# Kernel tuning notes

Hardware: AMD Instinct MI355X
Metric: run time of the kernel (lower is better)

Reference implementation:

```python
import jax, jax.numpy as jnp
from jax import lax
import numpy as np


def tropical_conv1d(x, w, padding, mode):
    """Tropical semiring conv1d.
    y[b,o,t] = sum_c reduce_k ( x[b,c,t+k] + w[o,c,k] )
    where reduce is min (min-plus) or max (max-plus). Zero padding like nn.Conv1d.
    x: [B, C, L], w: [O, C, K] -> y: [B, O, L + 2p - K + 1]
    """
    if padding:
        x = jnp.pad(x, ((0, 0), (0, 0), (padding, padding)))
    B, C, L = x.shape
    O, _, K = w.shape
    Lo = L - K + 1
    big = jnp.array(np.inf if mode == 'min' else -np.inf, dtype=x.dtype)
    acc0 = jnp.full((B, O, C, Lo), big, dtype=x.dtype)
    red = jnp.minimum if mode == 'min' else jnp.maximum
    wk_all = jnp.moveaxis(w, 2, 0)          # [K, O, C]
    ks = jnp.arange(K)

    def step(acc, inp):
        k, wk = inp
        xs = lax.dynamic_slice_in_dim(x, k, Lo, axis=2)      # [B, C, Lo]
        v = xs[:, None, :, :] + wk[None, :, :, None]          # [B, O, C, Lo]
        return red(acc, v), None

    acc, _ = lax.scan(step, acc0, (ks, wk_all))
    return acc.sum(axis=2)                                    # [B, O, Lo]


def avg_pool1d_2(x):
    # avg_pool1d(kernel=2, stride=2), truncating odd tail like torch
    B, C, L = x.shape
    Lh = L // 2
    return x[..., : Lh * 2].reshape(B, C, Lh, 2).mean(axis=-1)


def setup_inputs() -> dict:
    key = jax.random.key(0)
    ks = jax.random.split(key, 9)
    B, Cin, L = 64, 3, 8192
    linear_size = 32448
    s = lambda k, shape, fan: jax.random.normal(k, shape, dtype=jnp.float32) * (1.0 / np.sqrt(fan))
    return {
        'input': jax.random.normal(ks[0], (B, Cin, L), dtype=jnp.float32),
        'w1': s(ks[1], (6, Cin, 80), Cin * 80),
        'w2': s(ks[2], (16, 6, 3), 6 * 3),
        'fc1_w': s(ks[3], (120, linear_size), linear_size),
        'fc1_b': jnp.zeros((120,), jnp.float32),
        'fc2_w': s(ks[4], (84, 120), 120),
        'fc2_b': jnp.zeros((84,), jnp.float32),
        'fc3_w': s(ks[5], (10, 84), 84),
        'fc3_b': jnp.zeros((10,), jnp.float32),
    }


def reference(input, w1, w2, fc1_w, fc1_b, fc2_w, fc2_b, fc3_w, fc3_b):
    x = tropical_conv1d(input, w1, padding=2, mode='min')   # [B,6,L-75]
    x = avg_pool1d_2(x)
    x = tropical_conv1d(x, w2, padding=0, mode='max')       # [B,16,L2]
    x = avg_pool1d_2(x)
    x = x.reshape(x.shape[0], -1)                            # [B, 16*floor(L2/2)]
    x = jax.nn.relu(x @ fc1_w.T + fc1_b)
    x = jax.nn.relu(x @ fc2_w.T + fc2_b)
    return x @ fc3_w.T + fc3_b
```

## Files before the change

### kernel.cpp

```cpp
#include <hip/hip_runtime.h>

#define BB 64
#define C1 3
#define LIN 8192
#define PAD1 2
#define O1 6
#define KK1 80
#define LP1 4058

#define O2 16
#define KK2 3
#define LP2 2028

#define NFLAT 32448
#define H1 120
#define H2 84
#define NOUT 10

typedef _Float16 h2 __attribute__((ext_vector_type(2)));
typedef _Float16 f16x8 __attribute__((ext_vector_type(8)));
typedef float f32x4 __attribute__((ext_vector_type(4)));
#define BIGH ((_Float16)30000.0f)

__device__ __forceinline__ h2 bch2(float f) { return __builtin_bit_cast(h2, f); }
__device__ __forceinline__ h2 mkB(float nxt, float cur) {
  unsigned lo = __builtin_bit_cast(unsigned, cur);
  unsigned hi = __builtin_bit_cast(unsigned, nxt);
  return __builtin_bit_cast(h2, (lo >> 16) | (hi << 16));
}

__global__ __launch_bounds__(256) void k_prep(const float* __restrict__ w1,
                                              float* __restrict__ whb) {
  const int idx = threadIdx.x + blockIdx.x * 256;
  if (idx >= (O1 * C1) * (KK1 / 2)) return;
  const int oc = idx / (KK1 / 2);
  const int m  = idx - oc * (KK1 / 2);
  h2 v;
  v.x = (_Float16)w1[oc * KK1 + 2 * m];
  v.y = (_Float16)w1[oc * KK1 + 2 * m + 1];
  whb[idx] = __builtin_bit_cast(float, v);
}

#define TJ1 256
#define NT1 16
#define DWIN 297
#define DPAD 304

__global__ __launch_bounds__(512, 8) void k_conv1(const float* __restrict__ x,
                                                  const float* __restrict__ whb,
                                                  float* __restrict__ p1) {
  __shared__ float As[C1][DPAD];
  __shared__ float ws[O1 * C1 * 40];
  const int b    = blockIdx.x >> 4;
  const int tile = blockIdx.x & 15;
  const int j0   = tile * TJ1;
  const int tid  = threadIdx.x;

  for (int idx = tid; idx < O1 * C1 * 40; idx += 512) ws[idx] = whb[idx];
  for (int q = tid; q < C1 * DWIN; q += 512) {
    const int c = q / DWIN;
    const int d = q - c * DWIN;
    const int E = 2 * (j0 + d) - PAD1;
    const float* xc = x + ((size_t)b * C1 + c) * LIN;
    float f0 = 0.f, f1 = 0.f;
    if ((unsigned)E < LIN) f0 = xc[E];
    if ((unsigned)(E + 1) < LIN) f1 = xc[E + 1];
    h2 A; A.x = (_Float16)f0; A.y = (_Float16)f1;
    As[c][d] = __builtin_bit_cast(float, A);
  }
  __syncthreads();

  const int og = tid >> 8;
  const int jj = tid & 255;
  const int ob = og * 3;

  float r0 = 0.f, r1 = 0.f, r2 = 0.f;

  for (int c = 0; c < C1; ++c) {
    h2 aA[3], aB[3];
#pragma unroll
    for (int oo = 0; oo < 3; ++oo) {
      aA[oo].x = BIGH; aA[oo].y = BIGH;
      aB[oo].x = BIGH; aB[oo].y = BIGH;
    }
    float4 cur = *(const float4*)&As[c][jj];
#pragma unroll 2
    for (int mq = 0; mq < 10; ++mq) {
      float4 nxt = *(const float4*)&As[c][jj + 4 * mq + 4];
      h2 A0 = bch2(cur.x), A1 = bch2(cur.y), A2 = bch2(cur.z), A3 = bch2(cur.w);
      h2 B0 = mkB(cur.y, cur.x);
      h2 B1 = mkB(cur.z, cur.y);
      h2 B2 = mkB(cur.w, cur.z);
      h2 B3 = mkB(nxt.x, cur.w);
#pragma unroll
      for (int oo = 0; oo < 3; ++oo) {
        float4 wq = *(const float4*)&ws[((ob + oo) * C1 + c) * 40 + 4 * mq];
        h2 w0 = bch2(wq.x), w1v = bch2(wq.y), w2v = bch2(wq.z), w3v = bch2(wq.w);
        aA[oo] = __builtin_elementwise_min(aA[oo], A0 + w0);
        aB[oo] = __builtin_elementwise_min(aB[oo], B0 + w0);
        aA[oo] = __builtin_elementwise_min(aA[oo], A1 + w1v);
        aB[oo] = __builtin_elementwise_min(aB[oo], B1 + w1v);
        aA[oo] = __builtin_elementwise_min(aA[oo], A2 + w2v);
        aB[oo] = __builtin_elementwise_min(aB[oo], B2 + w2v);
        aA[oo] = __builtin_elementwise_min(aA[oo], A3 + w3v);
        aB[oo] = __builtin_elementwise_min(aB[oo], B3 + w3v);
      }
      cur = nxt;
    }
    r0 += fminf((float)aA[0].x, (float)aA[0].y) + fminf((float)aB[0].x, (float)aB[0].y);
    r1 += fminf((float)aA[1].x, (float)aA[1].y) + fminf((float)aB[1].x, (float)aB[1].y);
    r2 += fminf((float)aA[2].x, (float)aA[2].y) + fminf((float)aB[2].x, (float)aB[2].y);
  }

  const int j = j0 + jj;
  if (j < LP1) {
    float* pb = p1 + (size_t)b * O1 * LP1 + j;
    pb[(ob + 0) * LP1] = 0.5f * r0;
    pb[(ob + 1) * LP1] = 0.5f * r1;
    pb[(ob + 2) * LP1] = 0.5f * r2;
  }
}

#define T2 256
#define XT2 516

__global__ __launch_bounds__(256) void k_conv2(const float* __restrict__ p1,
                                               const float* __restrict__ w2,
                                               _Float16* __restrict__ p2h) {
  __shared__ float ps[O1][XT2];
  __shared__ float w2s[O2 * O1 * KK2];
  const int b    = blockIdx.x >> 3;
  const int tile = blockIdx.x & 7;
  const int j0   = tile * T2;
  const int tid  = threadIdx.x;

  for (int idx = tid; idx < O2 * O1 * KK2; idx += 256) w2s[idx] = w2[idx];
  for (int idx = tid; idx < O1 * XT2; idx += 256) {
    int c = idx / XT2;
    int p = idx - c * XT2;
    int t = 2 * j0 + p;
    ps[c][p] = (t < LP1) ? p1[((size_t)b * O1 + c) * LP1 + t] : 0.f;
  }
  __syncthreads();

  const int j = j0 + tid;
  if (j >= LP2) return;
  const int lb = 2 * tid;
  float xv[O1][4];
#pragma unroll
  for (int c = 0; c < O1; ++c) {
    xv[c][0] = ps[c][lb];     xv[c][1] = ps[c][lb + 1];
    xv[c][2] = ps[c][lb + 2]; xv[c][3] = ps[c][lb + 3];
  }
#pragma unroll
  for (int o = 0; o < O2; ++o) {
    float s = 0.f;
#pragma unroll
    for (int c = 0; c < O1; ++c) {
      float w0  = w2s[(o * O1 + c) * KK2 + 0];
      float w1v = w2s[(o * O1 + c) * KK2 + 1];
      float w2v = w2s[(o * O1 + c) * KK2 + 2];
      float m0 = fmaxf(fmaxf(xv[c][0] + w0, xv[c][1] + w1v), xv[c][2] + w2v);
      float m1 = fmaxf(fmaxf(xv[c][1] + w0, xv[c][2] + w1v), xv[c][3] + w2v);
      s += m0 + m1;
    }
    p2h[(size_t)b * NFLAT + o * LP2 + j] = (_Float16)(0.5f * s);
  }
}

#define KC2 64
#define NKC2 507

__global__ __launch_bounds__(256) void k_fc1(const _Float16* __restrict__ p2h,
                                             const float* __restrict__ w,
                                             _Float16* __restrict__ part) {
  __shared__ _Float16 bs[64][KC2];
  const int kc  = blockIdx.x;
  const int k0  = kc * KC2;
  const int tid = threadIdx.x;

#pragma unroll
  for (int r = 0; r < 2; ++r) {
    const int task = tid + 256 * r;
    const int row  = task >> 3;
    const int c4   = task & 7;
    float4 v = *(const float4*)&p2h[(size_t)row * NFLAT + k0 + c4 * 8];
    *(float4*)&bs[row][c4 * 8] = v;
  }
  __syncthreads();

  const int lane = tid & 63;
  const int wid  = tid >> 6;
  const int m_l  = lane & 15;
  const int q    = lane >> 4;
  const int m0   = wid * 32;

  const int rowA0 = m0 + m_l;
  int rowA1 = m0 + 16 + m_l;
  if (rowA1 > H1 - 1) rowA1 = H1 - 1;
  const float* wp0 = w + (size_t)rowA0 * NFLAT + k0 + q * 8;
  const float* wp1 = w + (size_t)rowA1 * NFLAT + k0 + q * 8;

  f32x4 acc[2][4];
#pragma unroll
  for (int t = 0; t < 2; ++t)
#pragma unroll
    for (int nt = 0; nt < 4; ++nt) acc[t][nt] = (f32x4){0.f, 0.f, 0.f, 0.f};

#pragma unroll
  for (int ks = 0; ks < 2; ++ks) {
    float4 a0l = *(const float4*)(wp0 + ks * 32);
    float4 a0h = *(const float4*)(wp0 + ks * 32 + 4);
    float4 a1l = *(const float4*)(wp1 + ks * 32);
    float4 a1h = *(const float4*)(wp1 + ks * 32 + 4);
    f16x8 A0, A1;
    A0[0] = (_Float16)a0l.x; A0[1] = (_Float16)a0l.y;
    A0[2] = (_Float16)a0l.z; A0[3] = (_Float16)a0l.w;
    A0[4] = (_Float16)a0h.x; A0[5] = (_Float16)a0h.y;
    A0[6] = (_Float16)a0h.z; A0[7] = (_Float16)a0h.w;
    A1[0] = (_Float16)a1l.x; A1[1] = (_Float16)a1l.y;
    A1[2] = (_Float16)a1l.z; A1[3] = (_Float16)a1l.w;
    A1[4] = (_Float16)a1h.x; A1[5] = (_Float16)a1h.y;
    A1[6] = (_Float16)a1h.z; A1[7] = (_Float16)a1h.w;
#pragma unroll
    for (int nt = 0; nt < 4; ++nt) {
      f16x8 Bf = *(const f16x8*)&bs[nt * 16 + m_l][ks * 32 + q * 8];
      acc[0][nt] = __builtin_amdgcn_mfma_f32_16x16x32_f16(A0, Bf, acc[0][nt], 0, 0, 0);
      acc[1][nt] = __builtin_amdgcn_mfma_f32_16x16x32_f16(A1, Bf, acc[1][nt], 0, 0, 0);
    }
  }

#pragma unroll
  for (int t = 0; t < 2; ++t)
#pragma unroll
    for (int nt = 0; nt < 4; ++nt)
#pragma unroll
      for (int r = 0; r < 4; ++r) {
        const int i = m0 + t * 16 + q * 4 + r;
        if (i < H1)
          part[((size_t)kc * H1 + i) * 64 + nt * 16 + m_l] = (_Float16)acc[t][nt][r];
      }
}

__global__ __launch_bounds__(512) void k_fc1red(const _Float16* __restrict__ part,
                                                float* __restrict__ part2) {
  __shared__ float red[512];
  const int bx  = blockIdx.x;
  const int s   = bx / H1;
  const int i   = bx - s * H1;
  const int tid = threadIdx.x;
  const int b   = tid & 63;
  const int sub = tid >> 6;
  const int kc0 = s * 127;
  const int kc1 = (kc0 + 127 < NKC2) ? kc0 + 127 : NKC2;
  float acc = 0.f;
  for (int kc = kc0 + sub; kc < kc1; kc += 8)
    acc += (float)part[((size_t)kc * H1 + i) * 64 + b];
  red[tid] = acc;
  __syncthreads();
  if (tid < 64) {
    float t = 0.f;
#pragma unroll
    for (int s2 = 0; s2 < 8; ++s2) t += red[b + 64 * s2];
    part2[((size_t)s * H1 + i) * 64 + b] = t;
  }
}

__global__ __launch_bounds__(128) void k_head(const float* __restrict__ part2,
                                              const float* __restrict__ fc1_b,
                                              const float* __restrict__ fc2_w,
                                              const float* __restrict__ fc2_b,
                                              const float* __restrict__ fc3_w,
                                              const float* __restrict__ fc3_b,
                                              float* __restrict__ out) {
  __shared__ float h1s[H1];
  __shared__ float h2s[H2];
  const int b = blockIdx.x;
  const int tid = threadIdx.x;
  if (tid < H1) {
    float v = part2[((size_t)0 * H1 + tid) * 64 + b]
            + part2[((size_t)1 * H1 + tid) * 64 + b]
            + part2[((size_t)2 * H1 + tid) * 64 + b]
            + part2[((size_t)3 * H1 + tid) * 64 + b];
    h1s[tid] = fmaxf(v + fc1_b[tid], 0.f);
  }
  __syncthreads();
  if (tid < H2) {
    float s = fc2_b[tid];
#pragma unroll 4
    for (int n = 0; n < H1; ++n) s += h1s[n] * fc2_w[tid * H1 + n];
    h2s[tid] = fmaxf(s, 0.f);
  }
  __syncthreads();
  if (tid < NOUT) {
    float s = fc3_b[tid];
#pragma unroll 4
    for (int n = 0; n < H2; ++n) s += h2s[n] * fc3_w[tid * H2 + n];
    out[b * NOUT + tid] = s;
  }
}

extern "C" void kernel_launch(void* const* d_in, const int* in_sizes, int n_in,
                              void* d_out, int out_size, void* d_ws, size_t ws_size,
                              hipStream_t stream) {
  const float* x     = (const float*)d_in[0];
  const float* w1    = (const float*)d_in[1];
  const float* w2    = (const float*)d_in[2];
  const float* fc1_w = (const float*)d_in[3];
  const float* fc1_b = (const float*)d_in[4];
  const float* fc2_w = (const float*)d_in[5];
  const float* fc2_b = (const float*)d_in[6];
  const float* fc3_w = (const float*)d_in[7];
  const float* fc3_b = (const float*)d_in[8];

  float* ws = (float*)d_ws;
  float*     p1    = ws;
  _Float16*  p2h   = (_Float16*)(p1 + (size_t)BB * O1 * LP1);
  _Float16*  part  = p2h + (size_t)BB * NFLAT;
  float*     part2 = (float*)(part + (size_t)NKC2 * H1 * 64);
  float*     whb   = part2 + (size_t)4 * H1 * 64;
  float*     out   = (float*)d_out;

  hipLaunchKernelGGL(k_prep, dim3(3), dim3(256), 0, stream, w1, whb);
  hipLaunchKernelGGL(k_conv1, dim3(BB * NT1), dim3(512), 0, stream, x, whb, p1);
  hipLaunchKernelGGL(k_conv2, dim3(BB * 8), dim3(256), 0, stream, p1, w2, p2h);
  hipLaunchKernelGGL(k_fc1, dim3(NKC2), dim3(256), 0, stream, p2h, fc1_w, part);
  hipLaunchKernelGGL(k_fc1red, dim3(4 * H1), dim3(512), 0, stream, part, part2);
  hipLaunchKernelGGL(k_head, dim3(BB), dim3(128), 0, stream, part2, fc1_b, fc2_w, fc2_b,
                     fc3_w, fc3_b, out);
}
```

Before: 146.5 us.

## Compute two output positions per thread in conv1 and use inline packed f16 asm

Each thread in the first tropical conv now handles two output positions 256 apart, so every weight load from shared memory serves twice as much work and the tile doubles to 512 columns with half as many blocks. The packed f16 add and min are issued through inline asm, and the tap loop is fully unrolled. The cost is higher register pressure (occupancy hint drops from 8 to 4), fewer blocks overall, and asm that may limit compiler scheduling.

```diff
diff --git a/kernel.cpp b/kernel.cpp
--- a/kernel.cpp
+++ b/kernel.cpp
@@ -23,10 +23,19 @@
 #define BIGH ((_Float16)30000.0f)
 
 __device__ __forceinline__ h2 bch2(float f) { return __builtin_bit_cast(h2, f); }
-__device__ __forceinline__ h2 mkB(float nxt, float cur) {
-  unsigned lo = __builtin_bit_cast(unsigned, cur);
-  unsigned hi = __builtin_bit_cast(unsigned, nxt);
-  return __builtin_bit_cast(h2, (lo >> 16) | (hi << 16));
+__device__ __forceinline__ unsigned bcu(float f) { return __builtin_bit_cast(unsigned, f); }
+__device__ __forceinline__ unsigned fsh(float nxt, float cur) {
+  return (bcu(cur) >> 16) | (bcu(nxt) << 16);
+}
+__device__ __forceinline__ unsigned pk_add(unsigned a, unsigned b) {
+  unsigned d;
+  asm("v_pk_add_f16 %0, %1, %2" : "=v"(d) : "v"(a), "v"(b));
+  return d;
+}
+__device__ __forceinline__ unsigned pk_min(unsigned a, unsigned b) {
+  unsigned d;
+  asm("v_pk_min_f16 %0, %1, %2" : "=v"(d) : "v"(a), "v"(b));
+  return d;
 }
 
 __global__ __launch_bounds__(256) void k_prep(const float* __restrict__ w1,
@@ -41,22 +50,23 @@
   whb[idx] = __builtin_bit_cast(float, v);
 }
 
-#define TJ1 256
-#define NT1 16
-#define DWIN 297
-#define DPAD 304
-
-__global__ __launch_bounds__(512, 8) void k_conv1(const float* __restrict__ x,
+#define TJ1 512
+#define NT1 8
+#define DWIN 555
+#define DPAD 560
+
+__global__ __launch_bounds__(512, 4) void k_conv1(const float* __restrict__ x,
                                                   const float* __restrict__ whb,
                                                   float* __restrict__ p1) {
   __shared__ float As[C1][DPAD];
-  __shared__ float ws[O1 * C1 * 40];
-  const int b    = blockIdx.x >> 4;
-  const int tile = blockIdx.x & 15;
+  __shared__ unsigned ws[O1 * C1 * 40];
+  const int b    = blockIdx.x >> 3;
+  const int tile = blockIdx.x & 7;
   const int j0   = tile * TJ1;
   const int tid  = threadIdx.x;
 
-  for (int idx = tid; idx < O1 * C1 * 40; idx += 512) ws[idx] = whb[idx];
+  for (int idx = tid; idx < O1 * C1 * 40; idx += 512)
+    ws[idx] = ((const unsigned*)whb)[idx];
   for (int q = tid; q < C1 * DWIN; q += 512) {
     const int c = q / DWIN;
     const int d = q - c * DWIN;
@@ -74,50 +84,63 @@
   const int jj = tid & 255;
   const int ob = og * 3;
 
-  float r0 = 0.f, r1 = 0.f, r2 = 0.f;
+  h2 binit; binit.x = BIGH; binit.y = BIGH;
+  const unsigned BIG2 = __builtin_bit_cast(unsigned, binit);
+
+  float r[2][3] = {{0.f, 0.f, 0.f}, {0.f, 0.f, 0.f}};
 
   for (int c = 0; c < C1; ++c) {
-    h2 aA[3], aB[3];
-#pragma unroll
-    for (int oo = 0; oo < 3; ++oo) {
-      aA[oo].x = BIGH; aA[oo].y = BIGH;
-      aB[oo].x = BIGH; aB[oo].y = BIGH;
+    unsigned aA[2][3], aB[2][3];
+#pragma unroll
+    for (int t = 0; t < 2; ++t)
+#pragma unroll
+      for (int oo = 0; oo < 3; ++oo) { aA[t][oo] = BIG2; aB[t][oo] = BIG2; }
+
+    float4 cur0 = *(const float4*)&As[c][jj];
+    float4 cur1 = *(const float4*)&As[c][jj + 256];
+#pragma unroll
+    for (int mq = 0; mq < 10; ++mq) {
+      float4 nxt0 = *(const float4*)&As[c][jj + 4 * mq + 4];
+      float4 nxt1 = *(const float4*)&As[c][jj + 256 + 4 * mq + 4];
+      unsigned A0[4] = {bcu(cur0.x), bcu(cur0.y), bcu(cur0.z), bcu(cur0.w)};
+      unsigned A1[4] = {bcu(cur1.x), bcu(cur1.y), bcu(cur1.z), bcu(cur1.w)};
+      unsigned B0[4] = {fsh(cur0.y, cur0.x), fsh(cur0.z, cur0.y),
+                        fsh(cur0.w, cur0.z), fsh(nxt0.x, cur0.w)};
+      unsigned B1[4] = {fsh(cur1.y, cur1.x), fsh(cur1.z, cur1.y),
+                        fsh(cur1.w, cur1.z), fsh(nxt1.x, cur1.w)};
+#pragma unroll
+      for (int oo = 0; oo < 3; ++oo) {
+        uint4 wq = *(const uint4*)&ws[((ob + oo) * C1 + c) * 40 + 4 * mq];
+        unsigned wv[4] = {wq.x, wq.y, wq.z, wq.w};
+#pragma unroll
+        for (int t = 0; t < 4; ++t) {
+          aA[0][oo] = pk_min(aA[0][oo], pk_add(A0[t], wv[t]));
+          aB[0][oo] = pk_min(aB[0][oo], pk_add(B0[t], wv[t]));
+          aA[1][oo] = pk_min(aA[1][oo], pk_add(A1[t], wv[t]));
+          aB[1][oo] = pk_min(aB[1][oo], pk_add(B1[t], wv[t]));
+        }
+      }
+      cur0 = nxt0; cur1 = nxt1;
     }
-    float4 cur = *(const float4*)&As[c][jj];
-#pragma unroll 2
-    for (int mq = 0; mq < 10; ++mq) {
-      float4 nxt = *(const float4*)&As[c][jj + 4 * mq + 4];
-      h2 A0 = bch2(cur.x), A1 = bch2(cur.y), A2 = bch2(cur.z), A3 = bch2(cur.w);
-      h2 B0 = mkB(cur.y, cur.x);
-      h2 B1 = mkB(cur.z, cur.y);
-      h2 B2 = mkB(cur.w, cur.z);
-      h2 B3 = mkB(nxt.x, cur.w);
+#pragma unroll
+    for (int t = 0; t < 2; ++t)
 #pragma unroll
       for (int oo = 0; oo < 3; ++oo) {
-        float4 wq = *(const float4*)&ws[((ob + oo) * C1 + c) * 40 + 4 * mq];
-        h2 w0 = bch2(wq.x), w1v = bch2(wq.y), w2v = bch2(wq.z), w3v = bch2(wq.w);
-        aA[oo] = __builtin_elementwise_min(aA[oo], A0 + w0);
-        aB[oo] = __builtin_elementwise_min(aB[oo], B0 + w0);
-        aA[oo] = __builtin_elementwise_min(aA[oo], A1 + w1v);
-        aB[oo] = __builtin_elementwise_min(aB[oo], B1 + w1v);
-        aA[oo] = __builtin_elementwise_min(aA[oo], A2 + w2v);
-        aB[oo] = __builtin_elementwise_min(aB[oo], B2 + w2v);
-        aA[oo] = __builtin_elementwise_min(aA[oo], A3 + w3v);
-        aB[oo] = __builtin_elementwise_min(aB[oo], B3 + w3v);
+        h2 va = __builtin_bit_cast(h2, aA[t][oo]);
+        h2 vb = __builtin_bit_cast(h2, aB[t][oo]);
+        r[t][oo] += fminf((float)va.x, (float)va.y) + fminf((float)vb.x, (float)vb.y);
       }
-      cur = nxt;
+  }
+
+#pragma unroll
+  for (int t = 0; t < 2; ++t) {
+    const int j = j0 + t * 256 + jj;
+    if (j < LP1) {
+      float* pb = p1 + (size_t)b * O1 * LP1 + j;
+      pb[(ob + 0) * LP1] = 0.5f * r[t][0];
+      pb[(ob + 1) * LP1] = 0.5f * r[t][1];
+      pb[(ob + 2) * LP1] = 0.5f * r[t][2];
     }
-    r0 += fminf((float)aA[0].x, (float)aA[0].y) + fminf((float)aB[0].x, (float)aB[0].y);
-    r1 += fminf((float)aA[1].x, (float)aA[1].y) + fminf((float)aB[1].x, (float)aB[1].y);
-    r2 += fminf((float)aA[2].x, (float)aA[2].y) + fminf((float)aB[2].x, (float)aB[2].y);
-  }
-
-  const int j = j0 + jj;
-  if (j < LP1) {
-    float* pb = p1 + (size_t)b * O1 * LP1 + j;
-    pb[(ob + 0) * LP1] = 0.5f * r0;
-    pb[(ob + 1) * LP1] = 0.5f * r1;
-    pb[(ob + 2) * LP1] = 0.5f * r2;
   }
 }
 
```

Measured after the change: 147.0 us. Within noise of the previous version (+0.3%).
